# Kernel optimization log

Hardware: AMD Instinct MI355X
Metric: run time of the kernel (lower is better)

The kernel has to match this reference:

```python
import jax, jax.numpy as jnp
import numpy as np

N, D0, D1, D2 = 8192, 512, 256, 64


def setup_inputs() -> dict:
    key = jax.random.key(0)
    k1, k2, k3, k4 = jax.random.split(key, 4)
    xi = jax.random.normal(k1, (N, D0), dtype=jnp.float32)
    # graph filter ~ row-normalized adjacency: nonnegative, entries O(1/N)
    filter_matrix = jax.random.uniform(k2, (N, N), dtype=jnp.float32) * (2.0 / N)
    b1 = np.sqrt(6.0 / (D0 + D1))
    b2 = np.sqrt(6.0 / (D1 + D2))
    w1 = jax.random.uniform(k3, (D0, D1), dtype=jnp.float32, minval=-b1, maxval=b1)
    w2 = jax.random.uniform(k4, (D1, D2), dtype=jnp.float32, minval=-b2, maxval=b2)
    return {"xi": xi, "filter_matrix": filter_matrix, "w1": w1, "w2": w2}


def reference(xi, filter_matrix, w1, w2):
    # two GCN layers: F @ (X @ W)
    h = jax.nn.relu(filter_matrix @ (xi @ w1))          # [N, D1]
    emb = filter_matrix @ (h @ w2)                       # [N, D2]
    # pairwise squared Euclidean distances between rows of emb -> [N, N]
    sq = jnp.sum(emb * emb, axis=1)                      # [N]
    dists = jnp.maximum(sq[:, None] + sq[None, :] - 2.0 * (emb @ emb.T), 0.0)
    recons_w = jax.nn.softmax(-dists, axis=1)            # row softmax of negative distances
    return emb, recons_w + 1e-10
```

## Files before the change

kernel.cpp:

```cpp
#include <hip/hip_runtime.h>

typedef short s16x8 __attribute__((ext_vector_type(8)));
typedef float f32x4 __attribute__((ext_vector_type(4)));
typedef unsigned int u32;

#define DEV static __device__ __forceinline__

DEV unsigned short f2bf(float x){
  u32 u = __builtin_bit_cast(u32, x);
  return (unsigned short)((u + 0x7FFFu + ((u >> 16) & 1u)) >> 16);
}
DEV float bf2f(unsigned short h){ u32 u = ((u32)h) << 16; return __builtin_bit_cast(float, u); }
DEV u32 pack2(float a, float b){ return (u32)f2bf(a) | ((u32)f2bf(b) << 16); }

DEV void gld16(const void* g, void* l){
  __builtin_amdgcn_global_load_lds((const __attribute__((address_space(1))) u32*)g,
                                   (__attribute__((address_space(3))) u32*)l, 16, 0, 0);
}

__global__ void k_transpose_bf16(const float* __restrict__ src,
                                 unsigned short* __restrict__ dst, int R, int C){
  int idx = blockIdx.x * 256 + threadIdx.x;
  if (idx >= R * C) return;
  int r = idx / C, c = idx % C;
  dst[(size_t)c * R + r] = f2bf(src[idx]);
}

template<int ROWS,int BK,int THREADS>
DEV void stage_lds_issue(const unsigned short* __restrict__ src, int row0, int ld,
                         int kk, char* lds, int tid){
  constexpr int SLOTS = BK/8, SLM = SLOTS-1, RPC = 64/SLOTS;
  constexpr int NCH = ROWS*BK*2/1024;
  constexpr int NW = THREADS/64, NI = NCH/NW;
  static_assert(NI*NW==NCH, "chunk exact");
  const int lane = tid & 63, wid = tid >> 6;
  #pragma unroll
  for (int i=0;i<NI;i++){
    int c = i*NW + wid;
    int r = c*RPC + lane/SLOTS;
    int s = lane & SLM;
    int ks = s ^ (r & SLM);
    gld16(src + (size_t)(row0+r)*ld + kk + ks*8, lds + c*1024);
  }
}

template<int ROWS,int BK,int THREADS,int NR>
DEV void stage_f32_load(const float* __restrict__ src, int row0, int ld, int kk,
                        float4* regs, int tid){
  #pragma unroll
  for (int i=0;i<NR;i++){
    int u = tid + i*THREADS;
    int r = u/(BK/4), c = u%(BK/4);
    regs[i] = *(const float4*)(src + (size_t)(row0+r)*ld + kk + c*4);
  }
}
template<int ROWS,int BK,int THREADS,int NR>
DEV void stage_f32_write(const float4* regs, char* lds, int tid){
  constexpr int SLM = BK/8 - 1;
  #pragma unroll
  for (int i=0;i<NR;i++){
    int u = tid + i*THREADS;
    int r = u/(BK/4), c = u%(BK/4);
    int2 p; p.x = (int)pack2(regs[i].x, regs[i].y);
            p.y = (int)pack2(regs[i].z, regs[i].w);
    int s = (c>>1) ^ (r & SLM);
    *(int2*)(lds + r*(BK*2) + s*16 + (c&1)*8) = p;
  }
}

template<int BM,int BN,int BK,int WR,int WC,bool AF32,bool BF32,bool ATOMIC>
__global__ __launch_bounds__(WR*WC*64)
void k_gemm_lds(const void* __restrict__ Ap, const void* __restrict__ Bp,
                void* __restrict__ Cp, int lda, int ldb, int ldc, int kchunk)
{
  constexpr int THREADS = WR*WC*64;
  constexpr int ROWB = BK*2, SLM = BK/8 - 1;
  constexpr int ABYTES = BM*ROWB, BBYTES = BN*ROWB;
  constexpr int WM = BM/WR, WN = BN/WC;
  constexpr int FM = WM/16, FN = WN/16, KS = BK/32;
  constexpr int NRA = AF32 ? BM*BK/(THREADS*4) : 1;
  constexpr int NRB = BF32 ? BN*BK/(THREADS*4) : 1;

  __shared__ char smem[2*(ABYTES+BBYTES)];
  char* A0 = smem; char* B0 = A0 + ABYTES;
  char* A1 = B0 + BBYTES; char* B1 = A1 + ABYTES;

  const int tid = threadIdx.x, lane = tid & 63;
  const int wid = tid >> 6, wrr = wid / WC, wcc = wid % WC;
  const int m0 = blockIdx.y * BM, n0 = blockIdx.x * BN;
  const int kbeg = blockIdx.z * kchunk, nk = kchunk / BK;

  const float* Af = (const float*)Ap;
  const unsigned short* Ah = (const unsigned short*)Ap;
  const float* Bf = (const float*)Bp;
  const unsigned short* Bh = (const unsigned short*)Bp;

  float4 areg[NRA], breg[NRB];

  f32x4 acc[FM][FN];
  f32x4 z4 = {0.f,0.f,0.f,0.f};
  #pragma unroll
  for (int m=0;m<FM;m++)
    #pragma unroll
    for (int n=0;n<FN;n++) acc[m][n] = z4;

  auto issue = [&](int kk, char* bA, char* bB){
    if constexpr (AF32) stage_f32_load<BM,BK,THREADS,NRA>(Af, m0, lda, kk, areg, tid);
    else                stage_lds_issue<BM,BK,THREADS>(Ah, m0, lda, kk, bA, tid);
    if constexpr (BF32) stage_f32_load<BN,BK,THREADS,NRB>(Bf, n0, ldb, kk, breg, tid);
    else                stage_lds_issue<BN,BK,THREADS>(Bh, n0, ldb, kk, bB, tid);
  };
  auto late_write = [&](char* bA, char* bB){
    if constexpr (AF32) stage_f32_write<BM,BK,THREADS,NRA>(areg, bA, tid);
    if constexpr (BF32) stage_f32_write<BN,BK,THREADS,NRB>(breg, bB, tid);
  };
  auto compute = [&](const char* bA, const char* bB){
    #pragma unroll
    for (int ks=0;ks<KS;ks++){
      s16x8 av[FM], bv[FN];
      #pragma unroll
      for (int m=0;m<FM;m++){
        int r = wrr*WM + m*16 + (lane&15);
        int s = (ks*4 + (lane>>4)) ^ (r & SLM);
        av[m] = *(const s16x8*)(bA + r*ROWB + s*16);
      }
      #pragma unroll
      for (int n=0;n<FN;n++){
        int r = wcc*WN + n*16 + (lane&15);
        int s = (ks*4 + (lane>>4)) ^ (r & SLM);
        bv[n] = *(const s16x8*)(bB + r*ROWB + s*16);
      }
      #pragma unroll
      for (int m=0;m<FM;m++)
        #pragma unroll
        for (int n=0;n<FN;n++)
          acc[m][n] = __builtin_amdgcn_mfma_f32_16x16x32_bf16(av[m], bv[n], acc[m][n], 0, 0, 0);
    }
  };

  issue(kbeg, A0, B0);
  late_write(A0, B0);
  __syncthreads();

  for (int t=0;t<nk;t++){
    char* cA = (t&1)?A1:A0; char* cB = (t&1)?B1:B0;
    char* nA = (t&1)?A0:A1; char* nB = (t&1)?B0:B1;
    bool pf = (t+1 < nk);
    if (pf) issue(kbeg + (t+1)*BK, nA, nB);
    compute(cA, cB);
    if (pf) late_write(nA, nB);
    __syncthreads();
  }

  if constexpr (ATOMIC) {
    float* Cf = (float*)Cp;
    #pragma unroll
    for (int m=0;m<FM;m++)
      #pragma unroll
      for (int n=0;n<FN;n++)
        #pragma unroll
        for (int r=0;r<4;r++){
          int row = m0 + wrr*WM + m*16 + (lane>>4)*4 + r;
          int col = n0 + wcc*WN + n*16 + (lane&15);
          atomicAdd(Cf + (size_t)row*ldc + col, acc[m][n][r]);
        }
  } else {
    unsigned short* Ch = (unsigned short*)Cp;
    #pragma unroll
    for (int m=0;m<FM;m++)
      #pragma unroll
      for (int n=0;n<FN;n++)
        #pragma unroll
        for (int r=0;r<4;r++){
          int row = m0 + wrr*WM + m*16 + (lane>>4)*4 + r;
          int col = n0 + wcc*WN + n*16 + (lane&15);
          Ch[(size_t)row*ldc + col] = f2bf(acc[m][n][r]);
        }
  }
}

__global__ void k_relu_bf16(const float* __restrict__ src, unsigned short* __restrict__ dst, int n4){
  int idx = blockIdx.x*256 + threadIdx.x;
  if (idx >= n4) return;
  float4 v = ((const float4*)src)[idx];
  int2 p;
  p.x = (int)pack2(fmaxf(v.x,0.f), fmaxf(v.y,0.f));
  p.y = (int)pack2(fmaxf(v.z,0.f), fmaxf(v.w,0.f));
  ((int2*)dst)[idx] = p;
}

__global__ void k_emb_fin(const float* __restrict__ acc, float* __restrict__ emb_out,
                          unsigned short* __restrict__ embb, float* __restrict__ sq){
  int idx = blockIdx.x*256 + threadIdx.x;
  float v = acc[idx];
  emb_out[idx] = v;
  unsigned short ub = f2bf(v);
  embb[idx] = ub;
  float x = bf2f(ub);
  float s = x*x;
  #pragma unroll
  for (int off=32; off>0; off>>=1) s += __shfl_xor(s, off, 64);
  if ((threadIdx.x & 63)==0) sq[idx>>6] = s;
}

template<int PASS>
__global__ __launch_bounds__(256)
void k_dist(const unsigned short* __restrict__ embb, const float* __restrict__ sq,
            float* __restrict__ S, float* __restrict__ out)
{
  constexpr int ROWB = 128, SLM = 7;
  __shared__ char smem[2*128*128];
  char* bufA = smem;
  char* bufB = smem + 128*ROWB;
  const int tid=threadIdx.x, lane=tid&63, wid=tid>>6;
  const int wrr = wid>>1, wcc = wid&1;
  const int i0 = blockIdx.y*128, j0 = blockIdx.x*128;

  #pragma unroll
  for (int i=0;i<4;i++){
    int u = tid + i*256;
    int r = u>>3, c = u&7;
    int byte = r*ROWB + ((c^(r&SLM))*16);
    *(int4*)(bufA+byte) = *(const int4*)(embb + (size_t)(i0+r)*64 + c*8);
    *(int4*)(bufB+byte) = *(const int4*)(embb + (size_t)(j0+r)*64 + c*8);
  }
  __syncthreads();

  f32x4 acc[4][4];
  f32x4 z4 = {0.f,0.f,0.f,0.f};
  #pragma unroll
  for (int m=0;m<4;m++)
    #pragma unroll
    for (int n=0;n<4;n++) acc[m][n]=z4;

  #pragma unroll
  for (int ks=0;ks<2;ks++){
    s16x8 av[4], bv[4];
    #pragma unroll
    for (int m=0;m<4;m++){
      int r = wrr*64 + m*16 + (lane&15);
      int slot = (ks*4 + (lane>>4)) ^ (r&SLM);
      av[m] = *(const s16x8*)(bufA + r*ROWB + slot*16);
    }
    #pragma unroll
    for (int n=0;n<4;n++){
      int r = wcc*64 + n*16 + (lane&15);
      int slot = (ks*4 + (lane>>4)) ^ (r&SLM);
      bv[n] = *(const s16x8*)(bufB + r*ROWB + slot*16);
    }
    #pragma unroll
    for (int m=0;m<4;m++)
      #pragma unroll
      for (int n=0;n<4;n++)
        acc[m][n] = __builtin_amdgcn_mfma_f32_16x16x32_bf16(av[m], bv[n], acc[m][n], 0, 0, 0);
  }

  float sqj[4];
  #pragma unroll
  for (int n=0;n<4;n++) sqj[n] = sq[j0 + wcc*64 + n*16 + (lane&15)];

  #pragma unroll
  for (int m=0;m<4;m++){
    #pragma unroll
    for (int r=0;r<4;r++){
      int row = i0 + wrr*64 + m*16 + (lane>>4)*4 + r;
      float sqi = sq[row];
      if constexpr (PASS==1){
        float v = 0.f;
        #pragma unroll
        for (int n=0;n<4;n++){
          float d = fmaxf(sqi + sqj[n] - 2.f*acc[m][n][r], 0.f);
          v += __expf(-d);
        }
        #pragma unroll
        for (int off=1; off<16; off<<=1) v += __shfl_xor(v, off, 64);
        if ((lane&15)==0) atomicAdd(S+row, v);
      } else {
        float inv = 1.0f / S[row];
        #pragma unroll
        for (int n=0;n<4;n++){
          int col = j0 + wcc*64 + n*16 + (lane&15);
          float d = fmaxf(sqi + sqj[n] - 2.f*acc[m][n][r], 0.f);
          out[(size_t)row*8192 + col] = __expf(-d)*inv + 1e-10f;
        }
      }
    }
  }
}

extern "C" void kernel_launch(void* const* d_in, const int* in_sizes, int n_in,
                              void* d_out, int out_size, void* d_ws, size_t ws_size,
                              hipStream_t stream)
{
  const float* xi = (const float*)d_in[0];
  const float* F  = (const float*)d_in[1];
  const float* w1 = (const float*)d_in[2];
  const float* w2 = (const float*)d_in[3];
  float* out = (float*)d_out;
  float* emb_out = out;
  float* recons  = out + (size_t)8192*64;

  char* ws = (char*)d_ws;
  size_t off = 0;
  auto alloc = [&](size_t bytes)->char*{ char* p = ws + off; off += (bytes + 255) & ~(size_t)255; return p; };
  unsigned short* w1t  = (unsigned short*)alloc((size_t)256*512*2);
  unsigned short* w2t  = (unsigned short*)alloc((size_t)64*256*2);
  unsigned short* t1t  = (unsigned short*)alloc((size_t)256*8192*2);
  unsigned short* h    = (unsigned short*)alloc((size_t)8192*256*2);
  unsigned short* t2t  = (unsigned short*)alloc((size_t)64*8192*2);
  unsigned short* embb = (unsigned short*)alloc((size_t)8192*64*2);
  float* sq    = (float*)alloc((size_t)8192*4);
  char* zbase = ws + off;
  float* h_acc   = (float*)alloc((size_t)8192*256*4);
  float* emb_acc = (float*)alloc((size_t)8192*64*4);
  float* S       = (float*)alloc((size_t)8192*4);
  size_t zbytes = (size_t)((ws + off) - zbase);

  hipMemsetAsync(zbase, 0, zbytes, stream);

  k_transpose_bf16<<<dim3((512*256+255)/256), 256, 0, stream>>>(w1, w1t, 512, 256);
  k_transpose_bf16<<<dim3((256*64+255)/256),  256, 0, stream>>>(w2, w2t, 256, 64);

  k_gemm_lds<128,64,64,2,2,false,true,false><<<dim3(128,2,1),256,0,stream>>>(
      w1t, xi, t1t, 512, 512, 8192, 512);

  k_gemm_lds<128,128,64,2,2,true,false,true><<<dim3(2,64,4),256,0,stream>>>(
      F, t1t, h_acc, 8192, 8192, 256, 2048);

  k_relu_bf16<<<dim3(8192*256/4/256),256,0,stream>>>(h_acc, h, 8192*256/4);

  k_gemm_lds<64,64,64,2,2,false,false,false><<<dim3(128,1,1),256,0,stream>>>(
      w2t, h, t2t, 256, 256, 8192, 256);

  k_gemm_lds<128,64,64,2,2,true,false,true><<<dim3(1,64,16),256,0,stream>>>(
      F, t2t, emb_acc, 8192, 8192, 64, 512);

  k_emb_fin<<<dim3(8192*64/256),256,0,stream>>>(emb_acc, emb_out, embb, sq);

  k_dist<1><<<dim3(64,64),256,0,stream>>>(embb, sq, S, recons);
  k_dist<2><<<dim3(64,64),256,0,stream>>>(embb, sq, S, recons);
}
```

Before: 356.8 us.

## Pre-convert filter and features to bf16, unify GEMM on async LDS loads

```diff
diff --git a/kernel.cpp b/kernel.cpp
--- a/kernel.cpp
+++ b/kernel.cpp
@@ -16,6 +16,16 @@
 DEV void gld16(const void* g, void* l){
   __builtin_amdgcn_global_load_lds((const __attribute__((address_space(1))) u32*)g,
                                    (__attribute__((address_space(3))) u32*)l, 16, 0, 0);
+}
+
+__global__ void k_cvt(const float* __restrict__ src, unsigned short* __restrict__ dst, long n4){
+  long i = (long)blockIdx.x*256 + threadIdx.x;
+  long stride = (long)gridDim.x*256;
+  for (; i < n4; i += stride){
+    float4 v = ((const float4*)src)[i];
+    int2 p; p.x = (int)pack2(v.x, v.y); p.y = (int)pack2(v.z, v.w);
+    ((int2*)dst)[i] = p;
+  }
 }
 
 __global__ void k_transpose_bf16(const float* __restrict__ src,
@@ -24,159 +34,6 @@
   if (idx >= R * C) return;
   int r = idx / C, c = idx % C;
   dst[(size_t)c * R + r] = f2bf(src[idx]);
-}
-
-template<int ROWS,int BK,int THREADS>
-DEV void stage_lds_issue(const unsigned short* __restrict__ src, int row0, int ld,
-                         int kk, char* lds, int tid){
-  constexpr int SLOTS = BK/8, SLM = SLOTS-1, RPC = 64/SLOTS;
-  constexpr int NCH = ROWS*BK*2/1024;
-  constexpr int NW = THREADS/64, NI = NCH/NW;
-  static_assert(NI*NW==NCH, "chunk exact");
-  const int lane = tid & 63, wid = tid >> 6;
-  #pragma unroll
-  for (int i=0;i<NI;i++){
-    int c = i*NW + wid;
-    int r = c*RPC + lane/SLOTS;
-    int s = lane & SLM;
-    int ks = s ^ (r & SLM);
-    gld16(src + (size_t)(row0+r)*ld + kk + ks*8, lds + c*1024);
-  }
-}
-
-template<int ROWS,int BK,int THREADS,int NR>
-DEV void stage_f32_load(const float* __restrict__ src, int row0, int ld, int kk,
-                        float4* regs, int tid){
-  #pragma unroll
-  for (int i=0;i<NR;i++){
-    int u = tid + i*THREADS;
-    int r = u/(BK/4), c = u%(BK/4);
-    regs[i] = *(const float4*)(src + (size_t)(row0+r)*ld + kk + c*4);
-  }
-}
-template<int ROWS,int BK,int THREADS,int NR>
-DEV void stage_f32_write(const float4* regs, char* lds, int tid){
-  constexpr int SLM = BK/8 - 1;
-  #pragma unroll
-  for (int i=0;i<NR;i++){
-    int u = tid + i*THREADS;
-    int r = u/(BK/4), c = u%(BK/4);
-    int2 p; p.x = (int)pack2(regs[i].x, regs[i].y);
-            p.y = (int)pack2(regs[i].z, regs[i].w);
-    int s = (c>>1) ^ (r & SLM);
-    *(int2*)(lds + r*(BK*2) + s*16 + (c&1)*8) = p;
-  }
-}
-
-template<int BM,int BN,int BK,int WR,int WC,bool AF32,bool BF32,bool ATOMIC>
-__global__ __launch_bounds__(WR*WC*64)
-void k_gemm_lds(const void* __restrict__ Ap, const void* __restrict__ Bp,
-                void* __restrict__ Cp, int lda, int ldb, int ldc, int kchunk)
-{
-  constexpr int THREADS = WR*WC*64;
-  constexpr int ROWB = BK*2, SLM = BK/8 - 1;
-  constexpr int ABYTES = BM*ROWB, BBYTES = BN*ROWB;
-  constexpr int WM = BM/WR, WN = BN/WC;
-  constexpr int FM = WM/16, FN = WN/16, KS = BK/32;
-  constexpr int NRA = AF32 ? BM*BK/(THREADS*4) : 1;
-  constexpr int NRB = BF32 ? BN*BK/(THREADS*4) : 1;
-
-  __shared__ char smem[2*(ABYTES+BBYTES)];
-  char* A0 = smem; char* B0 = A0 + ABYTES;
-  char* A1 = B0 + BBYTES; char* B1 = A1 + ABYTES;
-
-  const int tid = threadIdx.x, lane = tid & 63;
-  const int wid = tid >> 6, wrr = wid / WC, wcc = wid % WC;
-  const int m0 = blockIdx.y * BM, n0 = blockIdx.x * BN;
-  const int kbeg = blockIdx.z * kchunk, nk = kchunk / BK;
-
-  const float* Af = (const float*)Ap;
-  const unsigned short* Ah = (const unsigned short*)Ap;
-  const float* Bf = (const float*)Bp;
-  const unsigned short* Bh = (const unsigned short*)Bp;
-
-  float4 areg[NRA], breg[NRB];
-
-  f32x4 acc[FM][FN];
-  f32x4 z4 = {0.f,0.f,0.f,0.f};
-  #pragma unroll
-  for (int m=0;m<FM;m++)
-    #pragma unroll
-    for (int n=0;n<FN;n++) acc[m][n] = z4;
-
-  auto issue = [&](int kk, char* bA, char* bB){
-    if constexpr (AF32) stage_f32_load<BM,BK,THREADS,NRA>(Af, m0, lda, kk, areg, tid);
-    else                stage_lds_issue<BM,BK,THREADS>(Ah, m0, lda, kk, bA, tid);
-    if constexpr (BF32) stage_f32_load<BN,BK,THREADS,NRB>(Bf, n0, ldb, kk, breg, tid);
-    else                stage_lds_issue<BN,BK,THREADS>(Bh, n0, ldb, kk, bB, tid);
-  };
-  auto late_write = [&](char* bA, char* bB){
-    if constexpr (AF32) stage_f32_write<BM,BK,THREADS,NRA>(areg, bA, tid);
-    if constexpr (BF32) stage_f32_write<BN,BK,THREADS,NRB>(breg, bB, tid);
-  };
-  auto compute = [&](const char* bA, const char* bB){
-    #pragma unroll
-    for (int ks=0;ks<KS;ks++){
-      s16x8 av[FM], bv[FN];
-      #pragma unroll
-      for (int m=0;m<FM;m++){
-        int r = wrr*WM + m*16 + (lane&15);
-        int s = (ks*4 + (lane>>4)) ^ (r & SLM);
-        av[m] = *(const s16x8*)(bA + r*ROWB + s*16);
-      }
-      #pragma unroll
-      for (int n=0;n<FN;n++){
-        int r = wcc*WN + n*16 + (lane&15);
-        int s = (ks*4 + (lane>>4)) ^ (r & SLM);
-        bv[n] = *(const s16x8*)(bB + r*ROWB + s*16);
-      }
-      #pragma unroll
-      for (int m=0;m<FM;m++)
-        #pragma unroll
-        for (int n=0;n<FN;n++)
-          acc[m][n] = __builtin_amdgcn_mfma_f32_16x16x32_bf16(av[m], bv[n], acc[m][n], 0, 0, 0);
-    }
-  };
-
-  issue(kbeg, A0, B0);
-  late_write(A0, B0);
-  __syncthreads();
-
-  for (int t=0;t<nk;t++){
-    char* cA = (t&1)?A1:A0; char* cB = (t&1)?B1:B0;
-    char* nA = (t&1)?A0:A1; char* nB = (t&1)?B0:B1;
-    bool pf = (t+1 < nk);
-    if (pf) issue(kbeg + (t+1)*BK, nA, nB);
-    compute(cA, cB);
-    if (pf) late_write(nA, nB);
-    __syncthreads();
-  }
-
-  if constexpr (ATOMIC) {
-    float* Cf = (float*)Cp;
-    #pragma unroll
-    for (int m=0;m<FM;m++)
-      #pragma unroll
-      for (int n=0;n<FN;n++)
-        #pragma unroll
-        for (int r=0;r<4;r++){
-          int row = m0 + wrr*WM + m*16 + (lane>>4)*4 + r;
-          int col = n0 + wcc*WN + n*16 + (lane&15);
-          atomicAdd(Cf + (size_t)row*ldc + col, acc[m][n][r]);
-        }
-  } else {
-    unsigned short* Ch = (unsigned short*)Cp;
-    #pragma unroll
-    for (int m=0;m<FM;m++)
-      #pragma unroll
-      for (int n=0;n<FN;n++)
-        #pragma unroll
-        for (int r=0;r<4;r++){
-          int row = m0 + wrr*WM + m*16 + (lane>>4)*4 + r;
-          int col = n0 + wcc*WN + n*16 + (lane&15);
-          Ch[(size_t)row*ldc + col] = f2bf(acc[m][n][r]);
-        }
-  }
 }
 
 __global__ void k_relu_bf16(const float* __restrict__ src, unsigned short* __restrict__ dst, int n4){
@@ -187,6 +44,117 @@
   p.x = (int)pack2(fmaxf(v.x,0.f), fmaxf(v.y,0.f));
   p.y = (int)pack2(fmaxf(v.z,0.f), fmaxf(v.w,0.f));
   ((int2*)dst)[idx] = p;
+}
+
+template<int ROWS,int BK,int THREADS>
+DEV void stage_lds(const unsigned short* __restrict__ src, int row0, int ld,
+                   int kk, char* lds, int tid){
+  constexpr int SLOTS = BK/8, SLM = SLOTS-1, RPC = 64/SLOTS;
+  constexpr int NCH = ROWS*BK*2/1024;
+  constexpr int NW = THREADS/64, NI = NCH/NW;
+  static_assert(NI*NW==NCH, "chunk exact");
+  const int lane = tid & 63, wid = tid >> 6;
+  #pragma unroll
+  for (int i=0;i<NI;i++){
+    int c = i*NW + wid;
+    int r = c*RPC + lane/SLOTS;
+    int s = lane & SLM;
+    int ks = s ^ (r & SLM);
+    gld16(src + (size_t)(row0+r)*ld + kk + ks*8, lds + c*1024);
+  }
+}
+
+template<int BM,int BN,int BK,int WR,int WC,bool ATOMIC>
+__global__ __launch_bounds__(WR*WC*64)
+void k_gemm(const unsigned short* __restrict__ A, const unsigned short* __restrict__ B,
+            void* __restrict__ Cp, int lda, int ldb, int ldc, int kchunk)
+{
+  constexpr int THREADS = WR*WC*64;
+  constexpr int ROWB = BK*2, SLM = BK/8 - 1;
+  constexpr int ABYTES = BM*ROWB, BBYTES = BN*ROWB;
+  constexpr int WM = BM/WR, WN = BN/WC;
+  constexpr int FM = WM/16, FN = WN/16, KS = BK/32;
+
+  __shared__ char smem[2*(ABYTES+BBYTES)];
+  char* A0 = smem; char* B0 = A0 + ABYTES;
+  char* A1 = B0 + BBYTES; char* B1 = A1 + ABYTES;
+
+  const int tid = threadIdx.x, lane = tid & 63;
+  const int wid = tid >> 6, wrr = wid / WC, wcc = wid % WC;
+  const int m0 = blockIdx.y * BM, n0 = blockIdx.x * BN;
+  const int kbeg = blockIdx.z * kchunk, nk = kchunk / BK;
+
+  f32x4 acc[FM][FN];
+  f32x4 z4 = {0.f,0.f,0.f,0.f};
+  #pragma unroll
+  for (int m=0;m<FM;m++)
+    #pragma unroll
+    for (int n=0;n<FN;n++) acc[m][n] = z4;
+
+  auto issue = [&](int kk, char* bA, char* bB){
+    stage_lds<BM,BK,THREADS>(A, m0, lda, kk, bA, tid);
+    stage_lds<BN,BK,THREADS>(B, n0, ldb, kk, bB, tid);
+  };
+  auto compute = [&](const char* bA, const char* bB){
+    #pragma unroll
+    for (int ks=0;ks<KS;ks++){
+      s16x8 av[FM], bv[FN];
+      #pragma unroll
+      for (int m=0;m<FM;m++){
+        int r = wrr*WM + m*16 + (lane&15);
+        int s = (ks*4 + (lane>>4)) ^ (r & SLM);
+        av[m] = *(const s16x8*)(bA + r*ROWB + s*16);
+      }
+      #pragma unroll
+      for (int n=0;n<FN;n++){
+        int r = wcc*WN + n*16 + (lane&15);
+        int s = (ks*4 + (lane>>4)) ^ (r & SLM);
+        bv[n] = *(const s16x8*)(bB + r*ROWB + s*16);
+      }
+      #pragma unroll
+      for (int m=0;m<FM;m++)
+        #pragma unroll
+        for (int n=0;n<FN;n++)
+          acc[m][n] = __builtin_amdgcn_mfma_f32_16x16x32_bf16(av[m], bv[n], acc[m][n], 0, 0, 0);
+    }
+  };
+
+  issue(kbeg, A0, B0);
+  __syncthreads();
+
+  for (int t=0;t<nk;t++){
+    char* cA = (t&1)?A1:A0; char* cB = (t&1)?B1:B0;
+    char* nA = (t&1)?A0:A1; char* nB = (t&1)?B0:B1;
+    if (t+1 < nk) issue(kbeg + (t+1)*BK, nA, nB);
+    compute(cA, cB);
+    __syncthreads();
+  }
+
+  if constexpr (ATOMIC) {
+    float* Cf = (float*)Cp;
+    #pragma unroll
+    for (int m=0;m<FM;m++)
+      #pragma unroll
+      for (int n=0;n<FN;n++)
+        #pragma unroll
+        for (int r=0;r<4;r++){
+          int row = m0 + wrr*WM + m*16 + (lane>>4)*4 + r;
+          int col = n0 + wcc*WN + n*16 + (lane&15);
+          atomicAdd(Cf + (size_t)row*ldc + col, acc[m][n][r]);
+        }
+  } else {
+    unsigned short* Ch = (unsigned short*)Cp;
+    #pragma unroll
+    for (int m=0;m<FM;m++)
+      #pragma unroll
+      for (int n=0;n<FN;n++)
+        #pragma unroll
+        for (int r=0;r<4;r++){
+          int row = m0 + wrr*WM + m*16 + (lane>>4)*4 + r;
+          int col = n0 + wcc*WN + n*16 + (lane&15);
+          Ch[(size_t)row*ldc + col] = f2bf(acc[m][n][r]);
+        }
+  }
 }
 
 __global__ void k_emb_fin(const float* __restrict__ acc, float* __restrict__ emb_out,
@@ -300,14 +268,17 @@
   float* emb_out = out;
   float* recons  = out + (size_t)8192*64;
 
+  unsigned short* Fb = (unsigned short*)recons;
+
   char* ws = (char*)d_ws;
   size_t off = 0;
   auto alloc = [&](size_t bytes)->char*{ char* p = ws + off; off += (bytes + 255) & ~(size_t)255; return p; };
   unsigned short* w1t  = (unsigned short*)alloc((size_t)256*512*2);
   unsigned short* w2t  = (unsigned short*)alloc((size_t)64*256*2);
+  unsigned short* xib  = (unsigned short*)alloc((size_t)8192*512*2);
   unsigned short* t1t  = (unsigned short*)alloc((size_t)256*8192*2);
+  unsigned short* t2t  = (unsigned short*)alloc((size_t)64*8192*2);
   unsigned short* h    = (unsigned short*)alloc((size_t)8192*256*2);
-  unsigned short* t2t  = (unsigned short*)alloc((size_t)64*8192*2);
   unsigned short* embb = (unsigned short*)alloc((size_t)8192*64*2);
   float* sq    = (float*)alloc((size_t)8192*4);
   char* zbase = ws + off;
@@ -318,22 +289,24 @@
 
   hipMemsetAsync(zbase, 0, zbytes, stream);
 
+  k_cvt<<<dim3(2048),256,0,stream>>>(F,  Fb,  (long)8192*8192/4);
+  k_cvt<<<dim3(2048),256,0,stream>>>(xi, xib, (long)8192*512/4);
   k_transpose_bf16<<<dim3((512*256+255)/256), 256, 0, stream>>>(w1, w1t, 512, 256);
   k_transpose_bf16<<<dim3((256*64+255)/256),  256, 0, stream>>>(w2, w2t, 256, 64);
 
-  k_gemm_lds<128,64,64,2,2,false,true,false><<<dim3(128,2,1),256,0,stream>>>(
-      w1t, xi, t1t, 512, 512, 8192, 512);
-
-  k_gemm_lds<128,128,64,2,2,true,false,true><<<dim3(2,64,4),256,0,stream>>>(
-      F, t1t, h_acc, 8192, 8192, 256, 2048);
+  k_gemm<128,64,64,2,2,false><<<dim3(128,2,1),256,0,stream>>>(
+      w1t, xib, t1t, 512, 512, 8192, 512);
+
+  k_gemm<128,256,32,2,4,true><<<dim3(1,64,8),512,0,stream>>>(
+      Fb, t1t, h_acc, 8192, 8192, 256, 1024);
 
   k_relu_bf16<<<dim3(8192*256/4/256),256,0,stream>>>(h_acc, h, 8192*256/4);
 
-  k_gemm_lds<64,64,64,2,2,false,false,false><<<dim3(128,1,1),256,0,stream>>>(
+  k_gemm<64,64,64,2,2,false><<<dim3(128,1,1),256,0,stream>>>(
       w2t, h, t2t, 256, 256, 8192, 256);
 
-  k_gemm_lds<128,64,64,2,2,true,false,true><<<dim3(1,64,16),256,0,stream>>>(
-      F, t2t, emb_acc, 8192, 8192, 64, 512);
+  k_gemm<128,64,64,2,2,true><<<dim3(1,64,8),256,0,stream>>>(
+      Fb, t2t, emb_acc, 8192, 8192, 64, 1024);
 
   k_emb_fin<<<dim3(8192*64/256),256,0,stream>>>(emb_acc, emb_out, embb, sq);
 
```

After: 360.5 us. No clear change (+1.0%).
